# Kernel optimization log

Hardware: AMD Instinct MI355X
Metric: run time of the kernel (lower is better)

Reference implementation:

```python
import jax, jax.numpy as jnp
import numpy as np

B, T, D, H = 4096, 512, 1, 64

def _uniform(k, shape, scale):
    return jax.random.uniform(k, shape, jnp.float32, -scale, scale)

def setup_inputs() -> dict:
    key = jax.random.key(0)
    ks = jax.random.split(key, 12)
    s = 1.0 / np.sqrt(H)  # torch nn.LSTM init scale
    return {
        "x": jax.random.normal(ks[0], (B, T, D), jnp.float32),
        # layer 0 (input_size=D)
        "W_ih0": _uniform(ks[1], (4 * H, D), s),
        "W_hh0": _uniform(ks[2], (4 * H, H), s),
        "b_ih0": _uniform(ks[3], (4 * H,), s),
        "b_hh0": _uniform(ks[4], (4 * H,), s),
        # layer 1 (input_size=H)
        "W_ih1": _uniform(ks[5], (4 * H, H), s),
        "W_hh1": _uniform(ks[6], (4 * H, H), s),
        "b_ih1": _uniform(ks[7], (4 * H,), s),
        "b_hh1": _uniform(ks[8], (4 * H,), s),
        # final projection to scalar
        "W_fc": _uniform(ks[9], (1, H), s),
        "b_fc": _uniform(ks[10], (1,), s),
    }

def _lstm_layer(x_seq, W_ih, W_hh, b_ih, b_hh):
    # x_seq: (B, T, Din) -> hidden sequence (B, T, H). Gate order: i, f, g, o.
    b, t, _ = x_seq.shape
    h = W_hh.shape[1]
    # precompute input contribution for all timesteps: (T, B, 4H)
    x_proj = jnp.einsum('btd,gd->tbg', x_seq, W_ih) + b_ih + b_hh
    Whh_T = W_hh.T  # (H, 4H)

    def step(carry, xp):
        h_t, c_t = carry
        gates = xp + h_t @ Whh_T  # (B, 4H)
        i_g, f_g, g_g, o_g = jnp.split(gates, 4, axis=-1)
        i_g = jax.nn.sigmoid(i_g)
        f_g = jax.nn.sigmoid(f_g)
        g_g = jnp.tanh(g_g)
        o_g = jax.nn.sigmoid(o_g)
        c_t = f_g * c_t + i_g * g_g
        h_t = o_g * jnp.tanh(c_t)
        return (h_t, c_t), h_t

    h0 = jnp.zeros((b, h), x_seq.dtype)
    (_, _), hs = jax.lax.scan(step, (h0, h0), x_proj)  # hs: (T, B, H)
    return jnp.swapaxes(hs, 0, 1)

def reference(x, W_ih0, W_hh0, b_ih0, b_hh0, W_ih1, W_hh1, b_ih1, b_hh1, W_fc, b_fc):
    h1 = _lstm_layer(x, W_ih0, W_hh0, b_ih0, b_hh0)   # (B, T, H)
    h2 = _lstm_layer(h1, W_ih1, W_hh1, b_ih1, b_hh1)  # (B, T, H)
    last = h2[:, -1, :]                                # (B, H)
    return last @ W_fc.T + b_fc                        # (B, 1)
```

## Files before the change

kernel.cpp:

```cpp
#include <hip/hip_runtime.h>


#define TT 512
#define HH 64
#define NB 16
#define XP 516

typedef __bf16 bf16_t;
typedef bf16_t bf16x8 __attribute__((ext_vector_type(8)));
typedef float  f32x4  __attribute__((ext_vector_type(4)));
typedef float  f32x2  __attribute__((ext_vector_type(2)));

#define MFMA(A, B, C) __builtin_amdgcn_mfma_f32_16x16x32_bf16((A), (B), (C), 0, 0, 0)
#define RCPF(x) __builtin_amdgcn_rcpf(x)

#if __has_builtin(__builtin_amdgcn_exp2f)
#define EXP2F(x) __builtin_amdgcn_exp2f(x)
#else
__device__ __forceinline__ float EXP2F(float x) {
    float r;
    asm volatile("v_exp_f32 %0, %1" : "=v"(r) : "v"(x));
    return r;
}
#endif

#define SC_IFO (-1.4426950408889634f)
#define SC_G   ( 2.8853900817779268f)

__device__ __forceinline__ unsigned short f32_to_bf16_rne(float f) {
    unsigned int u = __builtin_bit_cast(unsigned int, f);
    unsigned int r = u + 0x7fffu + ((u >> 16) & 1u);
    return (unsigned short)(r >> 16);
}
__device__ __forceinline__ bf16_t bits_to_bf16(unsigned short u) {
    return __builtin_bit_cast(bf16_t, u);
}
__device__ __forceinline__ void build_frag_scaled(const float* __restrict__ p, float sc,
                                                  bf16x8& w) {
    const float4 a = *(const float4*)p;
    const float4 b = *(const float4*)(p + 4);
    float v[8] = {a.x, a.y, a.z, a.w, b.x, b.y, b.z, b.w};
#pragma unroll
    for (int jj = 0; jj < 8; ++jj)
        w[jj] = bits_to_bf16(f32_to_bf16_rne(v[jj] * sc));
}

__device__ __forceinline__ f32x2 exp2v(f32x2 v) {
    f32x2 r; r[0] = EXP2F(v[0]); r[1] = EXP2F(v[1]); return r;
}
__device__ __forceinline__ f32x2 rcpv(f32x2 v) {
    f32x2 r; r[0] = RCPF(v[0]); r[1] = RCPF(v[1]); return r;
}
__device__ __forceinline__ f32x2 cell2(const f32x4 a0, const f32x4 a1, f32x2* c) {
    f32x2 is = {a0[0], a1[0]}, fs = {a0[1], a1[1]};
    f32x2 gs = {a0[2], a1[2]}, os = {a0[3], a1[3]};
    const f32x2 pf = exp2v(fs);
    const f32x2 fg = rcpv(1.0f + pf);
    const f32x2 pi = exp2v(is);
    const f32x2 e2 = exp2v(gs);
    const f32x2 z  = (e2 - 1.0f) * rcpv((1.0f + pi) * (1.0f + e2));
    *c = fg * (*c) + z;
    const f32x2 po  = exp2v(os);
    const f32x2 e2c = exp2v((*c) * SC_G);
    return (e2c - 1.0f) * rcpv((1.0f + po) * (1.0f + e2c));
}

__device__ __forceinline__ int imin2(int a, int b) { return a < b ? a : b; }
__device__ __forceinline__ int min4of(const int* f) {
    const int4 v = *(const int4*)f;
    return imin2(imin2(v.x, v.y), imin2(v.z, v.w));
}
__device__ __forceinline__ int min8of(const int* f) {
    const int4 a = *(const int4*)f;
    const int4 b = *(const int4*)(f + 4);
    return imin2(imin2(imin2(a.x, a.y), imin2(a.z, a.w)),
                 imin2(imin2(b.x, b.y), imin2(b.z, b.w)));
}

__global__ __launch_bounds__(768, 3)
void lstm_1t_kernel(const float* __restrict__ x,
                    const float* __restrict__ Wih0, const float* __restrict__ Whh0,
                    const float* __restrict__ bih0, const float* __restrict__ bhh0,
                    const float* __restrict__ Wih1, const float* __restrict__ Whh1,
                    const float* __restrict__ bih1, const float* __restrict__ bhh1,
                    const float* __restrict__ Wfc,  const float* __restrict__ bfc,
                    float* __restrict__ out)
{
    __shared__ float xbuf[NB][XP];
    __shared__ unsigned short h0r[8][NB][64];
    __shared__ unsigned short h1r[2][NB][64];
    __shared__ float h1fin[HH][NB + 1];
    __shared__ __align__(16) int f0[4];
    __shared__ __align__(16) int f1[8];

    const int tid  = threadIdx.x;
    const int wv   = tid >> 6;
    const int lane = tid & 63;
    const int m    = lane & 15;
    const int q    = lane >> 4;
    const int m7   = m & 7;
    const int b0   = blockIdx.x * NB;
    const bool isL0 = (wv < 4);

    for (int i = tid; i < NB * TT / 4; i += 768) {
        const int b  = i >> 7;
        const int t4 = i & 127;
        *(float4*)&xbuf[b][t4 * 4] = *(const float4*)&x[(size_t)(b0 + b) * TT + t4 * 4];
    }
    for (int i = tid; i < 8 * NB * 64; i += 768) (&h0r[0][0][0])[i] = 0;
    for (int i = tid; i < 2 * NB * 64; i += 768) (&h1r[0][0][0])[i] = 0;
    if (tid < 4) f0[tid] = -1;
    else if (tid < 12) f1[tid - 4] = -1;

    int roff[2];
#pragma unroll
    for (int kt = 0; kt < 2; ++kt)
        roff[kt] = m * 64 + (((4 * kt + q) ^ m7) * 8);

    const int gate_m = m & 3;
    const float scA  = (gate_m == 2) ? SC_G : SC_IFO;
    unsigned short* const H0 = &h0r[0][0][0];
    unsigned short* const H1 = &h1r[0][0][0];

    __syncthreads();

    if (isL0) {
        const int w = wv;
        bf16x8 Ah[4][2];
        f32x4 bb0s[4], wx0s[4];
        int woff[4];
#pragma unroll
        for (int tau = 0; tau < 4; ++tau) {
            const int rowA = 64 * gate_m + 16 * w + 4 * tau + (m >> 2);
#pragma unroll
            for (int kt = 0; kt < 2; ++kt)
                build_frag_scaled(&Whh0[rowA * HH + kt * 32 + q * 8], scA, Ah[tau][kt]);
#pragma unroll
            for (int r = 0; r < 4; ++r) {
                const int row = 64 * r + 16 * w + 4 * tau + q;
                const float sc = (r == 2) ? SC_G : SC_IFO;
                bb0s[tau][r] = (bih0[row] + bhh0[row]) * sc;
                wx0s[tau][r] = Wih0[row] * sc;
            }
            const int u = 16 * w + 4 * tau + q;
            woff[tau] = m * 64 + (((u >> 3) ^ m7) * 8) + (u & 7);
        }

        f32x2 cA = {0.f, 0.f}, cB = {0.f, 0.f};

#pragma unroll 1
        for (int t = 0; t < TT; ++t) {
            while (min4of(f0) < t - 1) {
                asm volatile("" ::: "memory");
                __builtin_amdgcn_s_sleep(1);
            }
            asm volatile("" ::: "memory");

            const int rs = ((t - 1) & 7) * (NB * 64);
            bf16x8 h0[2];
            h0[0] = *(const bf16x8*)(H0 + rs + roff[0]);
            h0[1] = *(const bf16x8*)(H0 + rs + roff[1]);
            const float xv = xbuf[m][t];

            f32x4 a[4];
#pragma unroll
            for (int tau = 0; tau < 4; ++tau) {
                f32x4 p;
#pragma unroll
                for (int r = 0; r < 4; ++r)
                    p[r] = __builtin_fmaf(xv, wx0s[tau][r], bb0s[tau][r]);
                f32x4 z = {0.f, 0.f, 0.f, 0.f};
                p = MFMA(Ah[tau][0], h0[0], p);
                z = MFMA(Ah[tau][1], h0[1], z);
                a[tau] = p + z;
            }

            while (min8of(f1) < t - 8) {
                asm volatile("" ::: "memory");
                __builtin_amdgcn_s_sleep(1);
            }
            asm volatile("" ::: "memory");

            const f32x2 hv0 = cell2(a[0], a[1], &cA);
            const f32x2 hv1 = cell2(a[2], a[3], &cB);

            const int ws = (t & 7) * (NB * 64);
            H0[ws + woff[0]] = f32_to_bf16_rne(hv0[0]);
            H0[ws + woff[1]] = f32_to_bf16_rne(hv0[1]);
            H0[ws + woff[2]] = f32_to_bf16_rne(hv1[0]);
            H0[ws + woff[3]] = f32_to_bf16_rne(hv1[1]);

            asm volatile("s_waitcnt lgkmcnt(0)" ::: "memory");
            if (lane == 0) *(volatile int*)&f0[w] = t;
        }
    } else {
        const int uW = wv - 4;
        bf16x8 Ah[2][4];
        f32x4 bb1s[2];
        int woff[2], uu[2];
#pragma unroll
        for (int tau = 0; tau < 2; ++tau) {
            const int rowA = 64 * gate_m + 8 * uW + 4 * tau + (m >> 2);
#pragma unroll
            for (int kt = 0; kt < 2; ++kt)
                build_frag_scaled(&Wih1[rowA * HH + kt * 32 + q * 8], scA, Ah[tau][kt]);
#pragma unroll
            for (int kt = 0; kt < 2; ++kt)
                build_frag_scaled(&Whh1[rowA * HH + kt * 32 + q * 8], scA, Ah[tau][2 + kt]);
#pragma unroll
            for (int r = 0; r < 4; ++r) {
                const int row = 64 * r + 8 * uW + 4 * tau + q;
                const float sc = (r == 2) ? SC_G : SC_IFO;
                bb1s[tau][r] = (bih1[row] + bhh1[row]) * sc;
            }
            const int u = 8 * uW + 4 * tau + q;
            uu[tau]   = u;
            woff[tau] = m * 64 + (((u >> 3) ^ m7) * 8) + (u & 7);
        }

        f32x2 c1 = {0.f, 0.f};

#pragma unroll 1
        for (int t = 0; t < TT; ++t) {
            while (min4of(f0) < t) {
                asm volatile("" ::: "memory");
                __builtin_amdgcn_s_sleep(1);
            }
            asm volatile("" ::: "memory");
            const int rs0 = (t & 7) * (NB * 64);
            bf16x8 h0[2];
            h0[0] = *(const bf16x8*)(H0 + rs0 + roff[0]);
            h0[1] = *(const bf16x8*)(H0 + rs0 + roff[1]);

            while (min8of(f1) < t - 1) {
                asm volatile("" ::: "memory");
                __builtin_amdgcn_s_sleep(1);
            }
            asm volatile("" ::: "memory");
            const int rs1 = ((t - 1) & 1) * (NB * 64);
            bf16x8 h1[2];
            h1[0] = *(const bf16x8*)(H1 + rs1 + roff[0]);
            h1[1] = *(const bf16x8*)(H1 + rs1 + roff[1]);

            f32x4 a[2];
#pragma unroll
            for (int tau = 0; tau < 2; ++tau) {
                f32x4 p = bb1s[tau];
                f32x4 s = {0.f, 0.f, 0.f, 0.f};
                p = MFMA(Ah[tau][0], h0[0], p);
                p = MFMA(Ah[tau][1], h0[1], p);
                s = MFMA(Ah[tau][2], h1[0], s);
                s = MFMA(Ah[tau][3], h1[1], s);
                a[tau] = p + s;
            }

            const f32x2 hv = cell2(a[0], a[1], &c1);
            if (t == TT - 1) {
                h1fin[uu[0]][m] = hv[0];
                h1fin[uu[1]][m] = hv[1];
            }
            const int ws = (t & 1) * (NB * 64);
            H1[ws + woff[0]] = f32_to_bf16_rne(hv[0]);
            H1[ws + woff[1]] = f32_to_bf16_rne(hv[1]);

            asm volatile("s_waitcnt lgkmcnt(0)" ::: "memory");
            if (lane == 0) *(volatile int*)&f1[uW] = t;
        }
    }

    __syncthreads();

    if (tid < NB) {
        float sacc = bfc[0];
#pragma unroll
        for (int u = 0; u < HH; ++u) sacc = fmaf(h1fin[u][tid], Wfc[u], sacc);
        out[b0 + tid] = sacc;
    }
}

extern "C" void kernel_launch(void* const* d_in, const int* in_sizes, int n_in,
                              void* d_out, int out_size, void* d_ws, size_t ws_size,
                              hipStream_t stream) {
    const float* x    = (const float*)d_in[0];
    const float* Wih0 = (const float*)d_in[1];
    const float* Whh0 = (const float*)d_in[2];
    const float* bih0 = (const float*)d_in[3];
    const float* bhh0 = (const float*)d_in[4];
    const float* Wih1 = (const float*)d_in[5];
    const float* Whh1 = (const float*)d_in[6];
    const float* bih1 = (const float*)d_in[7];
    const float* bhh1 = (const float*)d_in[8];
    const float* Wfc  = (const float*)d_in[9];
    const float* bfc  = (const float*)d_in[10];

    lstm_1t_kernel<<<dim3(4096 / NB), dim3(768), 0, stream>>>(
        x, Wih0, Whh0, bih0, bhh0, Wih1, Whh1, bih1, bhh1, Wfc, bfc, (float*)d_out);
}
```

Baseline: 492.0 us.

## Fuse spin-wait flag checks and raise wave priority outside spin loops

```diff
diff --git a/kernel.cpp b/kernel.cpp
--- a/kernel.cpp
+++ b/kernel.cpp
@@ -76,6 +76,19 @@
     return imin2(imin2(imin2(a.x, a.y), imin2(a.z, a.w)),
                  imin2(imin2(b.x, b.y), imin2(b.z, b.w)));
 }
+
+#define SPIN_FUSED(F0, F1, C0, C1)                                              \
+    do {                                                                        \
+        __builtin_amdgcn_s_setprio(0);                                          \
+        for (;;) {                                                              \
+            asm volatile("" ::: "memory");                                      \
+            if ((min4of(F0) >= (C0)) & (min8of(F1) >= (C1))) break;             \
+            asm volatile("" ::: "memory");                                      \
+            if ((min4of(F0) >= (C0)) & (min8of(F1) >= (C1))) break;             \
+            __builtin_amdgcn_s_sleep(1);                                        \
+        }                                                                       \
+        __builtin_amdgcn_s_setprio(1);                                          \
+    } while (0)
 
 __global__ __launch_bounds__(768, 3)
 void lstm_1t_kernel(const float* __restrict__ x,
@@ -124,6 +137,8 @@
 
     __syncthreads();
 
+    __builtin_amdgcn_s_setprio(1);
+
     if (isL0) {
         const int w = wv;
         bf16x8 Ah[4][2];
@@ -150,36 +165,35 @@
 
 #pragma unroll 1
         for (int t = 0; t < TT; ++t) {
-            while (min4of(f0) < t - 1) {
-                asm volatile("" ::: "memory");
-                __builtin_amdgcn_s_sleep(1);
-            }
+            asm volatile("" ::: "memory");
+            const int c0 = t - 1;
+            const int c1 = t - 8;
+            const int rdy = (min4of(f0) >= c0) & (min8of(f1) >= c1);
+
+            const float xv = xbuf[m][t];
+            f32x4 a[4];
+#pragma unroll
+            for (int tau = 0; tau < 4; ++tau) {
+#pragma unroll
+                for (int r = 0; r < 4; ++r)
+                    a[tau][r] = __builtin_fmaf(xv, wx0s[tau][r], bb0s[tau][r]);
+            }
+
+            if (!rdy) SPIN_FUSED(f0, f1, c0, c1);
             asm volatile("" ::: "memory");
 
             const int rs = ((t - 1) & 7) * (NB * 64);
             bf16x8 h0[2];
             h0[0] = *(const bf16x8*)(H0 + rs + roff[0]);
             h0[1] = *(const bf16x8*)(H0 + rs + roff[1]);
-            const float xv = xbuf[m][t];
-
-            f32x4 a[4];
+
 #pragma unroll
             for (int tau = 0; tau < 4; ++tau) {
-                f32x4 p;
-#pragma unroll
-                for (int r = 0; r < 4; ++r)
-                    p[r] = __builtin_fmaf(xv, wx0s[tau][r], bb0s[tau][r]);
                 f32x4 z = {0.f, 0.f, 0.f, 0.f};
-                p = MFMA(Ah[tau][0], h0[0], p);
-                z = MFMA(Ah[tau][1], h0[1], z);
-                a[tau] = p + z;
-            }
-
-            while (min8of(f1) < t - 8) {
-                asm volatile("" ::: "memory");
-                __builtin_amdgcn_s_sleep(1);
-            }
-            asm volatile("" ::: "memory");
+                a[tau] = MFMA(Ah[tau][0], h0[0], a[tau]);
+                z      = MFMA(Ah[tau][1], h0[1], z);
+                a[tau] = a[tau] + z;
+            }
 
             const f32x2 hv0 = cell2(a[0], a[1], &cA);
             const f32x2 hv1 = cell2(a[2], a[3], &cB);
@@ -218,27 +232,22 @@
             woff[tau] = m * 64 + (((u >> 3) ^ m7) * 8) + (u & 7);
         }
 
-        f32x2 c1 = {0.f, 0.f};
+        f32x2 c1v = {0.f, 0.f};
 
 #pragma unroll 1
         for (int t = 0; t < TT; ++t) {
-            while (min4of(f0) < t) {
-                asm volatile("" ::: "memory");
-                __builtin_amdgcn_s_sleep(1);
-            }
             asm volatile("" ::: "memory");
+            const int c0 = t;
+            const int c1 = t - 1;
+            if (!((min4of(f0) >= c0) & (min8of(f1) >= c1)))
+                SPIN_FUSED(f0, f1, c0, c1);
+            asm volatile("" ::: "memory");
+
             const int rs0 = (t & 7) * (NB * 64);
-            bf16x8 h0[2];
+            const int rs1 = ((t - 1) & 1) * (NB * 64);
+            bf16x8 h0[2], h1[2];
             h0[0] = *(const bf16x8*)(H0 + rs0 + roff[0]);
             h0[1] = *(const bf16x8*)(H0 + rs0 + roff[1]);
-
-            while (min8of(f1) < t - 1) {
-                asm volatile("" ::: "memory");
-                __builtin_amdgcn_s_sleep(1);
-            }
-            asm volatile("" ::: "memory");
-            const int rs1 = ((t - 1) & 1) * (NB * 64);
-            bf16x8 h1[2];
             h1[0] = *(const bf16x8*)(H1 + rs1 + roff[0]);
             h1[1] = *(const bf16x8*)(H1 + rs1 + roff[1]);
 
@@ -254,7 +263,7 @@
                 a[tau] = p + s;
             }
 
-            const f32x2 hv = cell2(a[0], a[1], &c1);
+            const f32x2 hv = cell2(a[0], a[1], &c1v);
             if (t == TT - 1) {
                 h1fin[uu[0]][m] = hv[0];
                 h1fin[uu[1]][m] = hv[1];
```

New measurement: 492.4 us. About the same (+0.1%).
